# Optimization experiments

Hardware: AMD Instinct MI355X
Metric: run time of the kernel (lower is better)

Reference implementation:

```python
import jax, jax.numpy as jnp
import numpy as np

B, T, D, H = 1, 2048, 1024, 16
HD = D // H
STRIDE = T // 256  # hierarchical global stride (T > 512 branch)


def _mha(q_in, k_in, v_in, Wqkv, bqkv, Wo, bo, nh):
    """torch nn.MultiheadAttention (batch_first, eval/no-dropout), returns (out, head-avg attn)."""
    b, tq, d = q_in.shape
    hd = d // nh
    Wq, Wk, Wv = jnp.split(Wqkv, 3, axis=0)
    bq, bk, bv = jnp.split(bqkv, 3)
    def heads(x, W, bb):
        return (x @ W.T + bb).reshape(b, x.shape[1], nh, hd).transpose(0, 2, 1, 3)
    q = heads(q_in, Wq, bq)
    k = heads(k_in, Wk, bk)
    v = heads(v_in, Wv, bv)
    scores = jnp.einsum('bhtd,bhsd->bhts', q, k) / np.float32(np.sqrt(hd))
    attn = jax.nn.softmax(scores, axis=-1)
    out = jnp.einsum('bhts,bhsd->bhtd', attn, v).transpose(0, 2, 1, 3).reshape(b, tq, d)
    return out @ Wo.T + bo, attn.mean(axis=1)


def _interp_linear(x, size):
    """F.interpolate(mode='linear', align_corners=False) along axis 1. x: [B, Ts, C]."""
    ts = x.shape[1]
    src = (jnp.arange(size, dtype=x.dtype) + 0.5) * (ts / size) - 0.5
    src = jnp.clip(src, 0.0, ts - 1)
    i0 = jnp.floor(src).astype(jnp.int32)
    i1 = jnp.minimum(i0 + 1, ts - 1)
    w = (src - i0.astype(x.dtype))[None, :, None]
    return x[:, i0, :] * (1.0 - w) + x[:, i1, :] * w


def setup_inputs() -> dict:
    rng = jax.random.key(0)
    ks = iter(jax.random.split(rng, 32))
    s = 0.02
    n = lambda shape: jax.random.normal(next(ks), shape, dtype=jnp.float32) * s
    return {
        'query': jax.random.normal(next(ks), (B, T, D), jnp.float32),
        'key': jax.random.normal(next(ks), (B, T, D), jnp.float32),
        'value': jax.random.normal(next(ks), (B, T, D), jnp.float32),
        'strategy_probs': jax.nn.softmax(jax.random.normal(next(ks), (B, 4), jnp.float32), -1),
        'Wqkv_lin': n((3 * D, D)), 'b_lin': jnp.zeros((3 * D,), jnp.float32),
        'Wo_lin': n((D, D)), 'bo_lin': jnp.zeros((D,), jnp.float32),
        'sparsity_pattern': jax.random.normal(next(ks), (H, 1, 1), jnp.float32),
        'Wqkv_loc': n((3 * D, D)), 'b_loc': jnp.zeros((3 * D,), jnp.float32),
        'Wo_loc': n((D, D)), 'bo_loc': jnp.zeros((D,), jnp.float32),
        'Wqkv_glb': n((3 * D, D)), 'b_glb': jnp.zeros((3 * D,), jnp.float32),
        'Wo_glb': n((D, D)), 'bo_glb': jnp.zeros((D,), jnp.float32),
        'Wf': n((D, 2 * D)), 'bf': jnp.zeros((D,), jnp.float32),
        'R_quant': jax.random.normal(next(ks), (H, HD, HD), jnp.float32),
        'ent_gate': jax.random.normal(next(ks), (H, 2, 2), jnp.float32),
    }


def reference(query, key, value, strategy_probs, Wqkv_lin, b_lin, Wo_lin, bo_lin,
              sparsity_pattern, Wqkv_loc, b_loc, Wo_loc, bo_loc,
              Wqkv_glb, b_glb, Wo_glb, bo_glb, Wf, bf, R_quant, ent_gate):
    b, t, d = query.shape
    hd = d // H
    scale = np.float32(np.sqrt(hd))
    # --- 1) "linear" branch: standard MHA ---
    linear_out, linear_w = _mha(query, key, value, Wqkv_lin, b_lin, Wo_lin, bo_lin, H)
    # --- 2) sparse branch (per-head learned on/off mask on raw scores) ---
    qh = query.reshape(b, t, H, hd).transpose(0, 2, 1, 3)
    kh = key.reshape(b, t, H, hd).transpose(0, 2, 1, 3)
    vh = value.reshape(b, t, H, hd).transpose(0, 2, 1, 3)
    scores = jnp.einsum('bhtd,bhsd->bhts', qh, kh) / scale
    mask = (jax.nn.sigmoid(sparsity_pattern) > 0.5).astype(scores.dtype)  # [H,1,1]
    sp_attn = jax.nn.softmax(scores * mask[None], axis=-1)
    sparse_out = jnp.einsum('bhts,bhsd->bhtd', sp_attn, vh).transpose(0, 2, 1, 3).reshape(b, t, d)
    sparse_w = sp_attn.mean(axis=1)
    # --- 3) hierarchical branch (T > 512 path: strided global + linear interp) ---
    local_out, _ = _mha(query, key, value, Wqkv_loc, b_loc, Wo_loc, bo_loc, H // 2)
    gq, gk, gv = query[:, ::STRIDE], key[:, ::STRIDE], value[:, ::STRIDE]
    g_small, _ = _mha(gq, gk, gv, Wqkv_glb, b_glb, Wo_glb, bo_glb, H // 2)
    global_out = _interp_linear(g_small, t)
    hier_out = jnp.concatenate([local_out, global_out], axis=-1) @ Wf.T + bf
    # --- 4) quantum branch (per-head rotation + scalar gate on scores) ---
    q_rot = jnp.einsum('bhtd,hde->bhte', qh, R_quant)
    k_rot = jnp.einsum('bhtd,hde->bhte', kh, R_quant)
    gate = jax.nn.sigmoid(ent_gate[:, 0, 0])[None, :, None, None]  # [1,H,1,1]
    q_attn = jax.nn.softmax((jnp.einsum('bhtd,bhsd->bhts', q_rot, k_rot) / scale) * gate, axis=-1)
    quantum_out = jnp.einsum('bhts,bhsd->bhtd', q_attn, vh).transpose(0, 2, 1, 3).reshape(b, t, d)
    quantum_w = q_attn.mean(axis=1)
    # --- blend via strategy probabilities ---
    sp = strategy_probs[:, :, None]  # [B,4,1]
    all_out = jnp.stack([linear_out, sparse_out, hier_out, quantum_out], axis=1)  # [B,4,T,D]
    weighted = (all_out * sp[..., None]).sum(axis=1)  # [B,T,D]
    wstack = jnp.stack([linear_w, sparse_w, quantum_w], axis=1)  # [B,3,T,T]
    wsel = sp[:, jnp.array([0, 1, 3])][..., None, None]  # [B,3,1,1,1] (faithful to source; requires B==1)
    combined = (wstack * wsel).sum(axis=1)
    return weighted, combined
```

## Files before the change

### kernel.cpp

```cpp
#include <hip/hip_runtime.h>
#include <math.h>

#define D_MODEL 1024

typedef __attribute__((ext_vector_type(8))) short bf16x8;
typedef __attribute__((ext_vector_type(4))) float f32x4;
typedef __attribute__((ext_vector_type(8))) unsigned short u16x8;

__device__ __forceinline__ unsigned short bfr(float f) {
    unsigned u = __float_as_uint(f);
    u += 0x7fffu + ((u >> 16) & 1u);
    return (unsigned short)(u >> 16);
}
__device__ __forceinline__ float bff(unsigned short s) {
    return __uint_as_float(((unsigned)s) << 16);
}
__device__ __forceinline__ void split2(float x, unsigned short &h, unsigned short &l) {
    h = bfr(x);
    l = bfr(x - bff(h));
}
__device__ __forceinline__ unsigned cvtpk(float a, float b) {
    unsigned r;
    asm("v_cvt_pk_bf16_f32 %0, %1, %2" : "=v"(r) : "v"(a), "v"(b));
    return r;
}
__device__ __forceinline__ f32x4 mfma3(bf16x8 ah, bf16x8 al, bf16x8 bh, bf16x8 bl, f32x4 c) {
    c = __builtin_amdgcn_mfma_f32_16x16x32_bf16(ah, bh, c, 0, 0, 0);
    c = __builtin_amdgcn_mfma_f32_16x16x32_bf16(ah, bl, c, 0, 0, 0);
    c = __builtin_amdgcn_mfma_f32_16x16x32_bf16(al, bh, c, 0, 0, 0);
    return c;
}

__global__ __launch_bounds__(256) void split_rm(
    const float* __restrict__ in, unsigned short* __restrict__ hi,
    unsigned short* __restrict__ lo, int n4)
{
    int idx = blockIdx.x * 256 + threadIdx.x;
    if (idx >= n4) return;
    float4 v = ((const float4*)in)[idx];
    ushort4 hs, ls;
    split2(v.x, hs.x, ls.x); split2(v.y, hs.y, ls.y);
    split2(v.z, hs.z, ls.z); split2(v.w, hs.w, ls.w);
    ((ushort4*)hi)[idx] = hs;
    ((ushort4*)lo)[idx] = ls;
}

__global__ __launch_bounds__(256) void split_tr(
    const float* __restrict__ in, unsigned short* __restrict__ hi,
    unsigned short* __restrict__ lo, int T)
{
    __shared__ float xs[64][65];
    const int t0 = blockIdx.x * 64, d0 = blockIdx.y * 64;
    for (int idx = threadIdx.x; idx < 64 * 16; idx += 256) {
        int r = idx >> 4, c4 = (idx & 15) * 4;
        float4 v = *(const float4*)&in[(size_t)(t0 + r) * D_MODEL + d0 + c4];
        xs[r][c4] = v.x; xs[r][c4 + 1] = v.y; xs[r][c4 + 2] = v.z; xs[r][c4 + 3] = v.w;
    }
    __syncthreads();
    for (int idx = threadIdx.x; idx < 64 * 8; idx += 256) {
        int dd = idx >> 3, t8 = (idx & 7) * 8;
        u16x8 hs, ls;
#pragma unroll
        for (int j = 0; j < 8; ++j) {
            unsigned short hh, ll;
            split2(xs[t8 + j][dd], hh, ll);
            hs[j] = hh; ls[j] = ll;
        }
        *(u16x8*)&hi[(size_t)(d0 + dd) * T + t0 + t8] = hs;
        *(u16x8*)&lo[(size_t)(d0 + dd) * T + t0 + t8] = ls;
    }
}

__global__ __launch_bounds__(256) void gemm_mfma(
    const float* __restrict__ X0, const float* __restrict__ X1,
    const float* __restrict__ X2, int xrstride,
    const float* __restrict__ W, size_t wz, int wrstride,
    const float* __restrict__ bias, int bz,
    float* __restrict__ C, size_t cz, int M, int N, int K,
    const float* __restrict__ sptr, int sidx, int accum)
{
    const int z = blockIdx.z;
    const float* X = (z == 0) ? X0 : (z == 1 ? X1 : X2);
    W += (size_t)z * wz;
    if (bias) bias += z * bz;
    C += (size_t)z * cz;

    __shared__ unsigned short Xh[64][40], Xl[64][40];
    __shared__ unsigned short Wh[64][40], Wl[64][40];
    const int tid = threadIdx.x;
    const int m0 = blockIdx.x * 64, n0 = blockIdx.y * 64;
    const int lane = tid & 63, wave = tid >> 6;
    const int c = lane & 15, quad = lane >> 4;
    const int mbase = wave * 16;

    f32x4 acc[4];
#pragma unroll
    for (int nt = 0; nt < 4; ++nt) acc[nt] = (f32x4){0.f, 0.f, 0.f, 0.f};

    float4 xr[2], wr[2];
    const int r_ = tid >> 3, d4_ = (tid & 7) * 4;
    const int r2_ = (tid + 256) >> 3, d42_ = ((tid + 256) & 7) * 4;
    auto ldXW = [&](int k0) {
        xr[0] = *(const float4*)&X[(size_t)(m0 + r_) * xrstride + k0 + d4_];
        xr[1] = *(const float4*)&X[(size_t)(m0 + r2_) * xrstride + k0 + d42_];
        wr[0] = *(const float4*)&W[(size_t)(n0 + r_) * wrstride + k0 + d4_];
        wr[1] = *(const float4*)&W[(size_t)(n0 + r2_) * wrstride + k0 + d42_];
    };
    ldXW(0);

    for (int k0 = 0; k0 < K; k0 += 32) {
        __syncthreads();
        {
            ushort4 hs, ls;
            split2(xr[0].x, hs.x, ls.x); split2(xr[0].y, hs.y, ls.y);
            split2(xr[0].z, hs.z, ls.z); split2(xr[0].w, hs.w, ls.w);
            *(ushort4*)&Xh[r_][d4_] = hs; *(ushort4*)&Xl[r_][d4_] = ls;
            split2(xr[1].x, hs.x, ls.x); split2(xr[1].y, hs.y, ls.y);
            split2(xr[1].z, hs.z, ls.z); split2(xr[1].w, hs.w, ls.w);
            *(ushort4*)&Xh[r2_][d42_] = hs; *(ushort4*)&Xl[r2_][d42_] = ls;
            split2(wr[0].x, hs.x, ls.x); split2(wr[0].y, hs.y, ls.y);
            split2(wr[0].z, hs.z, ls.z); split2(wr[0].w, hs.w, ls.w);
            *(ushort4*)&Wh[r_][d4_] = hs; *(ushort4*)&Wl[r_][d4_] = ls;
            split2(wr[1].x, hs.x, ls.x); split2(wr[1].y, hs.y, ls.y);
            split2(wr[1].z, hs.z, ls.z); split2(wr[1].w, hs.w, ls.w);
            *(ushort4*)&Wh[r2_][d42_] = hs; *(ushort4*)&Wl[r2_][d42_] = ls;
        }
        __syncthreads();
        if (k0 + 32 < K) ldXW(k0 + 32);
        bf16x8 ah = *(const bf16x8*)&Xh[mbase + c][quad * 8];
        bf16x8 al = *(const bf16x8*)&Xl[mbase + c][quad * 8];
#pragma unroll
        for (int nt = 0; nt < 4; ++nt) {
            bf16x8 bh = *(const bf16x8*)&Wh[nt * 16 + c][quad * 8];
            bf16x8 bl = *(const bf16x8*)&Wl[nt * 16 + c][quad * 8];
            acc[nt] = mfma3(ah, al, bh, bl, acc[nt]);
        }
    }
    const float s = (sptr != nullptr) ? sptr[sidx] : 1.0f;
#pragma unroll
    for (int nt = 0; nt < 4; ++nt) {
#pragma unroll
        for (int reg = 0; reg < 4; ++reg) {
            int row = m0 + mbase + quad * 4 + reg;
            int col = n0 + nt * 16 + c;
            float v = acc[nt][reg] + (bias ? bias[col] : 0.0f);
            v *= s;
            size_t gi = (size_t)row * N + col;
            if (accum) v += C[gi];
            C[gi] = v;
        }
    }
}

template <int HD>
__global__ __launch_bounds__(256) void flash_mfma(
    const float* __restrict__ Q,
    const unsigned short* __restrict__ Khi, const unsigned short* __restrict__ Klo,
    const unsigned short* __restrict__ Vthi, const unsigned short* __restrict__ Vtlo,
    const float* __restrict__ aparam, int amode,
    float* __restrict__ O, float* __restrict__ O2,
    const float* __restrict__ strat, int o_sidx, int accum,
    float* __restrict__ mout, float* __restrict__ lout,
    int Tq, int Tk, float inv_scale)
{
    constexpr int ROWS = 64;
    constexpr int STILE = (HD == 64) ? 64 : 32;
    constexpr int MT   = STILE / 16;
    constexpr int KS   = HD / 32;
    constexpr int NT_O = HD / 16;
    constexpr int KS_PV = STILE / 32;
    constexpr bool SWZ = (HD == 64);
    constexpr int KPITCH = SWZ ? HD : HD + 8;
    constexpr int VPITCH = SWZ ? STILE : STILE + 8;
    constexpr int KIT = STILE * HD / 8 / 256;
    constexpr int VIT = STILE * HD / 8 / 256;

    __shared__ __align__(16) unsigned short Kh[STILE * KPITCH], Kl[STILE * KPITCH];
    __shared__ __align__(16) unsigned short Vh[HD * VPITCH],  Vl[HD * VPITCH];
    __shared__ __align__(16) unsigned short Ph[ROWS * VPITCH], Pl[ROWS * VPITCH];

    auto KIX = [](int r, int cc) {
        return SWZ ? r * HD + ((cc & 7) | ((((cc >> 3) ^ r) & 7) << 3))
                   : r * KPITCH + cc;
    };
    auto VIX = [](int d, int s) {
        return SWZ ? d * STILE + ((s & 7) | ((((s >> 3) ^ d) & 7) << 3))
                   : d * VPITCH + s;
    };
    auto PIX = [](int r, int cc) {
        return SWZ ? r * STILE + ((cc & 7) | ((((cc >> 3) ^ r) & 7) << 3))
                   : r * VPITCH + cc;
    };

    const int tid = threadIdx.x;
    const int h = blockIdx.y;
    const int r0 = blockIdx.x * ROWS;
    const int lane = tid & 63, wave = tid >> 6;
    const int c = lane & 15, quad = lane >> 4;
    const int mbase = wave * 16;
    const int ZS = gridDim.z;
    const int tkloc = Tk / ZS;
    const int kv0 = blockIdx.z * tkloc;

    float gate = 1.0f;
    if (amode == 1) gate = (aparam[h] > 0.0f) ? 1.0f : 0.0f;
    if (amode == 2) gate = 1.0f / (1.0f + __expf(-aparam[h * 4]));
    const float ascale = gate * inv_scale;
    const bool masked = (amode == 1) && (gate == 0.0f);

    bf16x8 qah[KS], qal[KS];
    if (!masked) {
        const float* qrow = &Q[(size_t)(r0 + mbase + c) * D_MODEL + h * HD];
#pragma unroll
        for (int ks = 0; ks < KS; ++ks) {
            float4 a  = *(const float4*)(qrow + ks * 32 + quad * 8);
            float4 b2 = *(const float4*)(qrow + ks * 32 + quad * 8 + 4);
            unsigned short hh, ll;
            split2(a.x, hh, ll);  qah[ks][0] = (short)hh; qal[ks][0] = (short)ll;
            split2(a.y, hh, ll);  qah[ks][1] = (short)hh; qal[ks][1] = (short)ll;
            split2(a.z, hh, ll);  qah[ks][2] = (short)hh; qal[ks][2] = (short)ll;
            split2(a.w, hh, ll);  qah[ks][3] = (short)hh; qal[ks][3] = (short)ll;
            split2(b2.x, hh, ll); qah[ks][4] = (short)hh; qal[ks][4] = (short)ll;
            split2(b2.y, hh, ll); qah[ks][5] = (short)hh; qal[ks][5] = (short)ll;
            split2(b2.z, hh, ll); qah[ks][6] = (short)hh; qal[ks][6] = (short)ll;
            split2(b2.w, hh, ll); qah[ks][7] = (short)hh; qal[ks][7] = (short)ll;
        }
    }

    float mreg = -1e30f, lacc = 0.0f;
    f32x4 oacc[NT_O];
#pragma unroll
    for (int nt = 0; nt < NT_O; ++nt) oacc[nt] = (f32x4){0.f, 0.f, 0.f, 0.f};

    bf16x8 pone, pzero;
#pragma unroll
    for (int j = 0; j < 8; ++j) { pone[j] = (short)0x3F80; pzero[j] = 0; }

    u16x8 krh[KIT], krl[KIT], vrh[VIT], vrl[VIT];

    auto load_regs = [&](int s0) {
        if (!masked) {
#pragma unroll
            for (int it = 0; it < KIT; ++it) {
                int idx = tid + it * 256;
                int r = idx / (HD / 8), c8 = (idx % (HD / 8)) * 8;
                size_t go = (size_t)(s0 + r) * D_MODEL + h * HD + c8;
                krh[it] = *(const u16x8*)&Khi[go];
                krl[it] = *(const u16x8*)&Klo[go];
            }
        }
#pragma unroll
        for (int it = 0; it < VIT; ++it) {
            int idx = tid + it * 256;
            int d = idx % HD, s8 = (idx / HD) * 8;
            size_t go = (size_t)(h * HD + d) * Tk + s0 + s8;
            vrh[it] = *(const u16x8*)&Vthi[go];
            vrl[it] = *(const u16x8*)&Vtlo[go];
        }
    };
    auto write_bufs = [&]() {
        if (!masked) {
#pragma unroll
            for (int it = 0; it < KIT; ++it) {
                int idx = tid + it * 256;
                int r = idx / (HD / 8), c8 = (idx % (HD / 8)) * 8;
                *(u16x8*)&Kh[KIX(r, c8)] = krh[it];
                *(u16x8*)&Kl[KIX(r, c8)] = krl[it];
            }
        }
#pragma unroll
        for (int it = 0; it < VIT; ++it) {
            int idx = tid + it * 256;
            int d = idx % HD, s8 = (idx / HD) * 8;
            *(u16x8*)&Vh[VIX(d, s8)] = vrh[it];
            *(u16x8*)&Vl[VIX(d, s8)] = vrl[it];
        }
    };

    auto compute_tile = [&]() {
        if (!masked) {
            f32x4 sf[MT];
#pragma unroll
            for (int mt = 0; mt < MT; ++mt) {
                f32x4 s = (f32x4){0.f, 0.f, 0.f, 0.f};
#pragma unroll
                for (int ks = 0; ks < KS; ++ks) {
                    bf16x8 kh = *(const bf16x8*)&Kh[KIX(mt * 16 + c, ks * 32 + quad * 8)];
                    bf16x8 kl = *(const bf16x8*)&Kl[KIX(mt * 16 + c, ks * 32 + quad * 8)];
                    s = mfma3(kh, kl, qah[ks], qal[ks], s);
                }
                sf[mt] = s * ascale;
            }
            float tm = sf[0][0];
#pragma unroll
            for (int mt = 0; mt < MT; ++mt)
#pragma unroll
                for (int reg = 0; reg < 4; ++reg) tm = fmaxf(tm, sf[mt][reg]);
            if (__any(tm > mreg + 8.0f)) {
                tm = fmaxf(tm, __shfl_xor(tm, 16));
                tm = fmaxf(tm, __shfl_xor(tm, 32));
                float nm = fmaxf(mreg, tm);
                float al = __expf(mreg - nm);
                mreg = nm;
                lacc *= al;
                float ar[4];
#pragma unroll
                for (int reg = 0; reg < 4; ++reg)
                    ar[reg] = __shfl(al, (lane & 48) | (quad * 4 + reg));
#pragma unroll
                for (int nt = 0; nt < NT_O; ++nt)
#pragma unroll
                    for (int reg = 0; reg < 4; ++reg) oacc[nt][reg] *= ar[reg];
            }
#pragma unroll
            for (int mt = 0; mt < MT; ++mt) {
                float p0 = __expf(sf[mt][0] - mreg);
                float p1 = __expf(sf[mt][1] - mreg);
                float p2 = __expf(sf[mt][2] - mreg);
                float p3 = __expf(sf[mt][3] - mreg);
                lacc += (p0 + p1) + (p2 + p3);
                unsigned h01 = cvtpk(p0, p1), h23 = cvtpk(p2, p3);
                float b0 = __uint_as_float(h01 << 16);
                float b1 = __uint_as_float(h01 & 0xffff0000u);
                float b2 = __uint_as_float(h23 << 16);
                float b3 = __uint_as_float(h23 & 0xffff0000u);
                unsigned l01 = cvtpk(p0 - b0, p1 - b1);
                unsigned l23 = cvtpk(p2 - b2, p3 - b3);
                uint2 hw; hw.x = h01; hw.y = h23;
                uint2 lw; lw.x = l01; lw.y = l23;
                *(uint2*)&Ph[PIX(mbase + c, mt * 16 + quad * 4)] = hw;
                *(uint2*)&Pl[PIX(mbase + c, mt * 16 + quad * 4)] = lw;
            }
        }
        bf16x8 pah[KS_PV], pal[KS_PV];
#pragma unroll
        for (int ks = 0; ks < KS_PV; ++ks) {
            if (masked) { pah[ks] = pone; pal[ks] = pzero; }
            else {
                pah[ks] = *(const bf16x8*)&Ph[PIX(mbase + c, ks * 32 + quad * 8)];
                pal[ks] = *(const bf16x8*)&Pl[PIX(mbase + c, ks * 32 + quad * 8)];
            }
        }
#pragma unroll
        for (int nt = 0; nt < NT_O; ++nt) {
            f32x4 o = oacc[nt];
#pragma unroll
            for (int ks = 0; ks < KS_PV; ++ks) {
                bf16x8 bh = *(const bf16x8*)&Vh[VIX(nt * 16 + c, ks * 32 + quad * 8)];
                bf16x8 bl = *(const bf16x8*)&Vl[VIX(nt * 16 + c, ks * 32 + quad * 8)];
                o = mfma3(pah[ks], pal[ks], bh, bl, o);
            }
            oacc[nt] = o;
        }
    };

    const int NTL = tkloc / STILE;
    load_regs(kv0);
    for (int t = 0; t < NTL; ++t) {
        __syncthreads();
        write_bufs();
        __syncthreads();
        if (t + 1 < NTL) load_regs(kv0 + (t + 1) * STILE);
        compute_tile();
    }

    lacc += __shfl_xor(lacc, 16);
    lacc += __shfl_xor(lacc, 32);

    if (ZS == 1) {
        const float osc = (o_sidx >= 0) ? strat[o_sidx] : 1.0f;
        if (quad == 0) {
            int row = r0 + mbase + c;
            mout[h * Tq + row] = masked ? 0.0f : mreg;
            lout[h * Tq + row] = masked ? (float)Tk : lacc;
        }
        float sc[4];
#pragma unroll
        for (int reg = 0; reg < 4; ++reg) {
            float lf = masked ? (float)Tk
                              : __shfl(lacc, (lane & 48) | (quad * 4 + reg));
            sc[reg] = osc / lf;
        }
#pragma unroll
        for (int reg = 0; reg < 4; ++reg) {
            int row = r0 + mbase + quad * 4 + reg;
#pragma unroll
            for (int nt = 0; nt < NT_O; ++nt) {
                size_t gi = (size_t)row * D_MODEL + h * HD + nt * 16 + c;
                float v = sc[reg] * oacc[nt][reg];
                if (accum) v += O[gi];
                O[gi] = v;
            }
        }
    } else {
        float* Op = (blockIdx.z == 0) ? O : O2;
        if (quad == 0) {
            int row = r0 + mbase + c;
            mout[(blockIdx.z * gridDim.y + h) * Tq + row] = masked ? 0.0f : mreg;
            lout[(blockIdx.z * gridDim.y + h) * Tq + row] = masked ? (float)tkloc : lacc;
        }
#pragma unroll
        for (int reg = 0; reg < 4; ++reg) {
            int row = r0 + mbase + quad * 4 + reg;
#pragma unroll
            for (int nt = 0; nt < NT_O; ++nt)
                Op[(size_t)row * D_MODEL + h * HD + nt * 16 + c] = oacc[nt][reg];
        }
    }
}

__global__ __launch_bounds__(256) void combineK(
    const float* __restrict__ O0, const float* __restrict__ O1,
    const float* __restrict__ mp, const float* __restrict__ lp,
    float* __restrict__ O, float* __restrict__ mf, float* __restrict__ lf,
    const float* __restrict__ strat, int o_sidx, int accum, int Tq,
    int hdshift, int NH)
{
    const int row = blockIdx.x;
    const int c4 = threadIdx.x * 4;
    const int h = c4 >> hdshift;
    const float m0 = mp[h * Tq + row], m1 = mp[(NH + h) * Tq + row];
    const float l0 = lp[h * Tq + row], l1 = lp[(NH + h) * Tq + row];
    const float m = fmaxf(m0, m1);
    const float w0 = __expf(m0 - m), w1 = __expf(m1 - m);
    const float lsum = l0 * w0 + l1 * w1;
    if (mf && (c4 & ((1 << hdshift) - 1)) == 0) {
        mf[h * Tq + row] = m;
        lf[h * Tq + row] = lsum;
    }
    const float osc = (o_sidx >= 0) ? strat[o_sidx] : 1.0f;
    const float sc = osc / lsum;
    float4 a = *(const float4*)&O0[(size_t)row * D_MODEL + c4];
    float4 b = *(const float4*)&O1[(size_t)row * D_MODEL + c4];
    size_t gi = (size_t)row * D_MODEL + c4;
    float4 r;
    r.x = sc * (a.x * w0 + b.x * w1);
    r.y = sc * (a.y * w0 + b.y * w1);
    r.z = sc * (a.z * w0 + b.z * w1);
    r.w = sc * (a.w * w0 + b.w * w1);
    if (accum) {
        float4 o = *(const float4*)&O[gi];
        r.x += o.x; r.y += o.y; r.z += o.z; r.w += o.w;
    }
    *(float4*)&O[gi] = r;
}

__global__ __launch_bounds__(256) void comb_mfma(
    const unsigned short* __restrict__ Qhi, const unsigned short* __restrict__ Qlo,
    const unsigned short* __restrict__ Khi, const unsigned short* __restrict__ Klo,
    const float* __restrict__ mrow, const float* __restrict__ lrow,
    const float* __restrict__ aparam, int amode,
    const float* __restrict__ strat,
    float* __restrict__ comb, int Tq, int Tk, int nh, float inv_scale)
{
    __shared__ __align__(16) unsigned short Kh[128][72], Kl[128][72];
    __shared__ float msh[16 * 64], lsh[16 * 64];
    const int tid = threadIdx.x;
    const int r0 = blockIdx.x * 64, c0 = blockIdx.y * 128;
    const int lane = tid & 63, wave = tid >> 6;
    const int c = lane & 15, quad = lane >> 4;
    const int mbase = wave * 16;

    for (int idx = tid; idx < nh * 64; idx += 256) {
        int hh = idx >> 6, rr = idx & 63;
        msh[idx] = mrow[hh * Tq + r0 + rr];
        lsh[idx] = 1.0f / lrow[hh * Tq + r0 + rr];
    }

    f32x4 acc[8];
#pragma unroll
    for (int nt = 0; nt < 8; ++nt) acc[nt] = (f32x4){0.f, 0.f, 0.f, 0.f};

    int hlist[16]; float glist[16]; int nact = 0; float unif = 0.0f;
    for (int h = 0; h < nh; ++h) {
        float gate = 1.0f;
        if (amode == 1) gate = (aparam[h] > 0.0f) ? 1.0f : 0.0f;
        if (amode == 2) gate = 1.0f / (1.0f + __expf(-aparam[h * 4]));
        if (amode == 1 && gate == 0.0f) { unif += 1.0f; continue; }
        hlist[nact] = h; glist[nact] = gate * inv_scale; ++nact;
    }

    u16x8 krh[4], krl[4];
    auto loadK = [&](int h) {
#pragma unroll
        for (int it = 0; it < 4; ++it) {
            int idx = tid + it * 256;
            int r = idx >> 3, c8 = (idx & 7) * 8;
            size_t go = (size_t)(c0 + r) * D_MODEL + h * 64 + c8;
            krh[it] = *(const u16x8*)&Khi[go];
            krl[it] = *(const u16x8*)&Klo[go];
        }
    };
    if (nact > 0) loadK(hlist[0]);

    for (int i = 0; i < nact; ++i) {
        const int h = hlist[i];
        const float ascale = glist[i];
        __syncthreads();
#pragma unroll
        for (int it = 0; it < 4; ++it) {
            int idx = tid + it * 256;
            int r = idx >> 3, c8 = (idx & 7) * 8;
            *(u16x8*)&Kh[r][c8] = krh[it];
            *(u16x8*)&Kl[r][c8] = krl[it];
        }
        __syncthreads();
        if (i + 1 < nact) loadK(hlist[i + 1]);

        bf16x8 qah[2], qal[2];
        const unsigned short* qh = &Qhi[(size_t)(r0 + mbase + c) * D_MODEL + h * 64];
        const unsigned short* ql = &Qlo[(size_t)(r0 + mbase + c) * D_MODEL + h * 64];
#pragma unroll
        for (int ks = 0; ks < 2; ++ks) {
            qah[ks] = *(const bf16x8*)(qh + ks * 32 + quad * 8);
            qal[ks] = *(const bf16x8*)(ql + ks * 32 + quad * 8);
        }

        float mr[4], li[4];
#pragma unroll
        for (int reg = 0; reg < 4; ++reg) {
            mr[reg] = msh[h * 64 + mbase + quad * 4 + reg];
            li[reg] = lsh[h * 64 + mbase + quad * 4 + reg];
        }
#pragma unroll
        for (int nt = 0; nt < 8; ++nt) {
            f32x4 s = (f32x4){0.f, 0.f, 0.f, 0.f};
#pragma unroll
            for (int ks = 0; ks < 2; ++ks) {
                bf16x8 bh = *(const bf16x8*)&Kh[nt * 16 + c][ks * 32 + quad * 8];
                bf16x8 bl = *(const bf16x8*)&Kl[nt * 16 + c][ks * 32 + quad * 8];
                s = mfma3(qah[ks], qal[ks], bh, bl, s);
            }
#pragma unroll
            for (int reg = 0; reg < 4; ++reg)
                acc[nt][reg] += __expf(s[reg] * ascale - mr[reg]) * li[reg];
        }
    }
    const float csc = (strat[0] + strat[1] + strat[3]) / (float)nh;
    const float uadd = unif / (float)Tk;
#pragma unroll
    for (int nt = 0; nt < 8; ++nt) {
#pragma unroll
        for (int reg = 0; reg < 4; ++reg) {
            int row = r0 + mbase + quad * 4 + reg;
            comb[(size_t)row * Tk + c0 + nt * 16 + c] = csc * (acc[nt][reg] + uadd);
        }
    }
}

__global__ __launch_bounds__(256) void rotate_heads(
    const float* __restrict__ X0, const float* __restrict__ X1,
    const float* __restrict__ R,
    float* __restrict__ Y0, float* __restrict__ Y1)
{
    const float* X = blockIdx.z ? X1 : X0;
    float* Y = blockIdx.z ? Y1 : Y0;
    __shared__ float Rt[64][68];
    __shared__ float xs[64][68];
    const int tid = threadIdx.x;
    const int h = blockIdx.y;
    const int t0 = blockIdx.x * 64;
    for (int idx = tid; idx < 4096; idx += 256) {
        int d = idx >> 6, e = idx & 63;
        Rt[e][d] = R[h * 4096 + idx];
        xs[d][e] = X[(size_t)(t0 + d) * D_MODEL + h * 64 + e];
    }
    __syncthreads();
    const int ty = tid >> 4, tx = tid & 15;
    float acc[4][4] = {};
#pragma unroll 4
    for (int d0 = 0; d0 < 64; d0 += 4) {
        float4 rv[4];
#pragma unroll
        for (int j = 0; j < 4; ++j) rv[j] = *(const float4*)&Rt[tx * 4 + j][d0];
#pragma unroll
        for (int i = 0; i < 4; ++i) {
            float4 a = *(const float4*)&xs[ty * 4 + i][d0];
#pragma unroll
            for (int j = 0; j < 4; ++j)
                acc[i][j] += a.x * rv[j].x + a.y * rv[j].y + a.z * rv[j].z + a.w * rv[j].w;
        }
    }
#pragma unroll
    for (int i = 0; i < 4; ++i)
#pragma unroll
        for (int j = 0; j < 4; ++j)
            Y[(size_t)(t0 + ty * 4 + i) * D_MODEL + h * 64 + tx * 4 + j] = acc[i][j];
}

__global__ __launch_bounds__(256) void interp_lin(
    const float* __restrict__ G, float* __restrict__ out)
{
    const int t = blockIdx.x;
    float src = (t + 0.5f) * 0.125f - 0.5f;
    src = fminf(fmaxf(src, 0.0f), 255.0f);
    float fl = floorf(src);
    int i0 = (int)fl;
    int i1 = min(i0 + 1, 255);
    float w = src - fl;
    const float4* g0 = (const float4*)(G + (size_t)i0 * D_MODEL);
    const float4* g1 = (const float4*)(G + (size_t)i1 * D_MODEL);
    float4* o = (float4*)(out + (size_t)t * D_MODEL);
    int c = threadIdx.x;
    float4 a = g0[c], b = g1[c];
    float4 r;
    r.x = a.x * (1.0f - w) + b.x * w;
    r.y = a.y * (1.0f - w) + b.y * w;
    r.z = a.z * (1.0f - w) + b.z * w;
    r.w = a.w * (1.0f - w) + b.w * w;
    o[c] = r;
}

extern "C" void kernel_launch(void* const* d_in, const int* in_sizes, int n_in,
                              void* d_out, int out_size, void* d_ws, size_t ws_size,
                              hipStream_t stream)
{
    (void)in_sizes; (void)n_in; (void)ws_size; (void)out_size;
    const float* query    = (const float*)d_in[0];
    const float* key      = (const float*)d_in[1];
    const float* value    = (const float*)d_in[2];
    const float* strat    = (const float*)d_in[3];
    const float* Wqkv_lin = (const float*)d_in[4];
    const float* b_lin    = (const float*)d_in[5];
    const float* Wo_lin   = (const float*)d_in[6];
    const float* bo_lin   = (const float*)d_in[7];
    const float* spars    = (const float*)d_in[8];
    const float* Wqkv_loc = (const float*)d_in[9];
    const float* b_loc    = (const float*)d_in[10];
    const float* Wo_loc   = (const float*)d_in[11];
    const float* bo_loc   = (const float*)d_in[12];
    const float* Wqkv_glb = (const float*)d_in[13];
    const float* b_glb    = (const float*)d_in[14];
    const float* Wo_glb   = (const float*)d_in[15];
    const float* bo_glb   = (const float*)d_in[16];
    const float* Wf       = (const float*)d_in[17];
    const float* bf       = (const float*)d_in[18];
    const float* Rq       = (const float*)d_in[19];
    const float* ent      = (const float*)d_in[20];

    float* out = (float*)d_out;
    float* weighted = out;
    float* combined = out + (size_t)2048 * 1024;
    const size_t PLANE = (size_t)2048 * 2048;

    float* ws   = (float*)d_ws;
    float* qkv  = ws;
    float* AO   = qkv + 6291456;
    float* LO   = AO + 2097152;
    float* gqkv = LO + 2097152;
    float* gAO  = gqkv + 786432;
    float* gOUT = gAO + 262144;
    float* GI   = gOUT + 262144;
    float* mb   = GI + 2097152;
    float* lb   = mb + 65536;
    float* qrot = qkv;
    float* krot = qkv + 2097152;
    unsigned short* Ksp_h = (unsigned short*)(lb + 65536);
    unsigned short* Ksp_l = Ksp_h + 2097152;
    unsigned short* Vtp_h = Ksp_l + 2097152;
    unsigned short* Vtp_l = Vtp_h + 2097152;
    unsigned short* gKs_h = Vtp_l + 2097152;
    unsigned short* gKs_l = gKs_h + 262144;
    unsigned short* gVt_h = gKs_l + 262144;
    unsigned short* gVt_l = gVt_h + 262144;
    float* mc = (float*)(gVt_l + 262144);
    float* lc = mc + 32768;
    unsigned short* Qsp_h = (unsigned short*)GI;
    unsigned short* Qsp_l = Qsp_h + 2097152;

    const float inv8   = 0.125f;
    const float inv128 = 1.0f / sqrtf(128.0f);

    hipMemsetAsync(weighted, 0, (size_t)2097152 * sizeof(float), stream);

    gemm_mfma<<<dim3(32, 16, 3), 256, 0, stream>>>(
        query, key, value, 1024, Wqkv_lin, 1048576, 1024, b_lin, 1024,
        qkv, 2097152, 2048, 1024, 1024, nullptr, 0, 0);
    split_rm<<<dim3(2048), 256, 0, stream>>>(qkv + 2097152, Ksp_h, Ksp_l, 524288);
    split_tr<<<dim3(32, 16), 256, 0, stream>>>(qkv + 4194304, Vtp_h, Vtp_l, 2048);
    flash_mfma<64><<<dim3(32, 16, 2), 256, 0, stream>>>(
        qkv, Ksp_h, Ksp_l, Vtp_h, Vtp_l, nullptr, 0,
        AO, GI, strat, -1, 0, mb, lb, 2048, 2048, inv8);
    combineK<<<dim3(2048), 256, 0, stream>>>(
        AO, GI, mb, lb, AO, mc, lc, strat, -1, 0, 2048, 6, 16);
    split_rm<<<dim3(2048), 256, 0, stream>>>(qkv, Qsp_h, Qsp_l, 524288);
    comb_mfma<<<dim3(32, 16), 256, 0, stream>>>(
        Qsp_h, Qsp_l, Ksp_h, Ksp_l, mc, lc, nullptr, 0, strat,
        combined + 0 * PLANE, 2048, 2048, 16, inv8);
    gemm_mfma<<<dim3(32, 16, 1), 256, 0, stream>>>(
        AO, AO, AO, 1024, Wo_lin, 0, 1024, bo_lin, 0,
        weighted, 0, 2048, 1024, 1024, strat, 0, 1);

    split_rm<<<dim3(2048), 256, 0, stream>>>(key, Ksp_h, Ksp_l, 524288);
    split_tr<<<dim3(32, 16), 256, 0, stream>>>(value, Vtp_h, Vtp_l, 2048);
    flash_mfma<64><<<dim3(32, 16, 2), 256, 0, stream>>>(
        query, Ksp_h, Ksp_l, Vtp_h, Vtp_l, spars, 1,
        AO, GI, strat, 1, 1, mb, lb, 2048, 2048, inv8);
    combineK<<<dim3(2048), 256, 0, stream>>>(
        AO, GI, mb, lb, weighted, mc, lc, strat, 1, 1, 2048, 6, 16);
    split_rm<<<dim3(2048), 256, 0, stream>>>(query, Qsp_h, Qsp_l, 524288);
    comb_mfma<<<dim3(32, 16), 256, 0, stream>>>(
        Qsp_h, Qsp_l, Ksp_h, Ksp_l, mc, lc, spars, 1, strat,
        combined + 1 * PLANE, 2048, 2048, 16, inv8);

    rotate_heads<<<dim3(32, 16, 2), 256, 0, stream>>>(query, key, Rq, qrot, krot);
    split_rm<<<dim3(2048), 256, 0, stream>>>(krot, Ksp_h, Ksp_l, 524288);
    flash_mfma<64><<<dim3(32, 16, 2), 256, 0, stream>>>(
        qrot, Ksp_h, Ksp_l, Vtp_h, Vtp_l, ent, 2,
        AO, GI, strat, 3, 1, mb, lb, 2048, 2048, inv8);
    combineK<<<dim3(2048), 256, 0, stream>>>(
        AO, GI, mb, lb, weighted, mc, lc, strat, 3, 1, 2048, 6, 16);
    split_rm<<<dim3(2048), 256, 0, stream>>>(qrot, Qsp_h, Qsp_l, 524288);
    comb_mfma<<<dim3(32, 16), 256, 0, stream>>>(
        Qsp_h, Qsp_l, Ksp_h, Ksp_l, mc, lc, ent, 2, strat,
        combined + 2 * PLANE, 2048, 2048, 16, inv8);

    gemm_mfma<<<dim3(32, 16, 3), 256, 0, stream>>>(
        query, key, value, 1024, Wqkv_loc, 1048576, 1024, b_loc, 1024,
        qkv, 2097152, 2048, 1024, 1024, nullptr, 0, 0);
    split_rm<<<dim3(2048), 256, 0, stream>>>(qkv + 2097152, Ksp_h, Ksp_l, 524288);
    split_tr<<<dim3(32, 16), 256, 0, stream>>>(qkv + 4194304, Vtp_h, Vtp_l, 2048);
    flash_mfma<128><<<dim3(32, 8, 2), 256, 0, stream>>>(
        qkv, Ksp_h, Ksp_l, Vtp_h, Vtp_l, nullptr, 0,
        AO, GI, strat, -1, 0, mb, lb, 2048, 2048, inv128);
    combineK<<<dim3(2048), 256, 0, stream>>>(
        AO, GI, mb, lb, AO, nullptr, nullptr, strat, -1, 0, 2048, 7, 8);
    gemm_mfma<<<dim3(32, 16, 1), 256, 0, stream>>>(
        AO, AO, AO, 1024, Wo_loc, 0, 1024, bo_loc, 0,
        LO, 0, 2048, 1024, 1024, nullptr, 0, 0);

    gemm_mfma<<<dim3(4, 16, 3), 256, 0, stream>>>(
        query, key, value, 8192, Wqkv_glb, 1048576, 1024, b_glb, 1024,
        gqkv, 262144, 256, 1024, 1024, nullptr, 0, 0);
    split_rm<<<dim3(256), 256, 0, stream>>>(gqkv + 262144, gKs_h, gKs_l, 65536);
    split_tr<<<dim3(4, 16), 256, 0, stream>>>(gqkv + 524288, gVt_h, gVt_l, 256);
    flash_mfma<128><<<dim3(4, 8, 1), 256, 0, stream>>>(
        gqkv, gKs_h, gKs_l, gVt_h, gVt_l, nullptr, 0,
        gAO, nullptr, strat, -1, 0, mb, lb, 256, 256, inv128);
    gemm_mfma<<<dim3(4, 16, 1), 256, 0, stream>>>(
        gAO, gAO, gAO, 1024, Wo_glb, 0, 1024, bo_glb, 0,
        gOUT, 0, 256, 1024, 1024, nullptr, 0, 0);
    interp_lin<<<dim3(2048), 256, 0, stream>>>(gOUT, GI);

    gemm_mfma<<<dim3(32, 16, 1), 256, 0, stream>>>(
        LO, LO, LO, 1024, Wf, 0, 2048, bf, 0,
        weighted, 0, 2048, 1024, 1024, strat, 2, 1);
    gemm_mfma<<<dim3(32, 16, 1), 256, 0, stream>>>(
        GI, GI, GI, 1024, Wf + 1024, 0, 2048, nullptr, 0,
        weighted, 0, 2048, 1024, 1024, strat, 2, 1);
}
```

Before: 1.078 ms.

## Pre-split GEMM operands into bf16 hi/lo once and reuse across branches

The GEMM kernel now loads pre-split bf16 hi/lo operands instead of fp32 data that it had to split into hi/lo inside every tile iteration. Query, key and value are split once and the results are shared by the three QKV projections, and also stand in for the separate key/query splits in the sparse branch. Weights and activations are split by extra split_rm launches before each GEMM. This removes redundant per-tile conversion work but adds several kernel launches and extra global traffic to write and read the split buffers.

New measurement: 1.035 ms. 1.04x faster.

```diff
diff --git a/kernel.cpp b/kernel.cpp
--- a/kernel.cpp
+++ b/kernel.cpp
@@ -71,22 +71,26 @@
     }
 }
 
-__global__ __launch_bounds__(256) void gemm_mfma(
-    const float* __restrict__ X0, const float* __restrict__ X1,
-    const float* __restrict__ X2, int xrstride,
-    const float* __restrict__ W, size_t wz, int wrstride,
+__global__ __launch_bounds__(256) void gemm_bf(
+    const unsigned short* __restrict__ Xh0, const unsigned short* __restrict__ Xl0,
+    const unsigned short* __restrict__ Xh1, const unsigned short* __restrict__ Xl1,
+    const unsigned short* __restrict__ Xh2, const unsigned short* __restrict__ Xl2,
+    int xrstride,
+    const unsigned short* __restrict__ Whi, const unsigned short* __restrict__ Wlo,
+    size_t wz, int wrstride,
     const float* __restrict__ bias, int bz,
     float* __restrict__ C, size_t cz, int M, int N, int K,
     const float* __restrict__ sptr, int sidx, int accum)
 {
     const int z = blockIdx.z;
-    const float* X = (z == 0) ? X0 : (z == 1 ? X1 : X2);
-    W += (size_t)z * wz;
+    const unsigned short* Xh_g = (z == 0) ? Xh0 : (z == 1 ? Xh1 : Xh2);
+    const unsigned short* Xl_g = (z == 0) ? Xl0 : (z == 1 ? Xl1 : Xl2);
+    Whi += (size_t)z * wz; Wlo += (size_t)z * wz;
     if (bias) bias += z * bz;
     C += (size_t)z * cz;
 
-    __shared__ unsigned short Xh[64][40], Xl[64][40];
-    __shared__ unsigned short Wh[64][40], Wl[64][40];
+    __shared__ __align__(16) unsigned short Xh[64][40], Xl[64][40];
+    __shared__ __align__(16) unsigned short Wh[64][40], Wl[64][40];
     const int tid = threadIdx.x;
     const int m0 = blockIdx.x * 64, n0 = blockIdx.y * 64;
     const int lane = tid & 63, wave = tid >> 6;
@@ -97,36 +101,26 @@
 #pragma unroll
     for (int nt = 0; nt < 4; ++nt) acc[nt] = (f32x4){0.f, 0.f, 0.f, 0.f};
 
-    float4 xr[2], wr[2];
-    const int r_ = tid >> 3, d4_ = (tid & 7) * 4;
-    const int r2_ = (tid + 256) >> 3, d42_ = ((tid + 256) & 7) * 4;
-    auto ldXW = [&](int k0) {
-        xr[0] = *(const float4*)&X[(size_t)(m0 + r_) * xrstride + k0 + d4_];
-        xr[1] = *(const float4*)&X[(size_t)(m0 + r2_) * xrstride + k0 + d42_];
-        wr[0] = *(const float4*)&W[(size_t)(n0 + r_) * wrstride + k0 + d4_];
-        wr[1] = *(const float4*)&W[(size_t)(n0 + r2_) * wrstride + k0 + d42_];
+    const int r_ = tid >> 2, c8_ = (tid & 3) * 8;
+    u16x8 xh, xl, wh, wl;
+    auto ld = [&](int k0) {
+        size_t xo = (size_t)(m0 + r_) * xrstride + k0 + c8_;
+        xh = *(const u16x8*)&Xh_g[xo];
+        xl = *(const u16x8*)&Xl_g[xo];
+        size_t wo = (size_t)(n0 + r_) * wrstride + k0 + c8_;
+        wh = *(const u16x8*)&Whi[wo];
+        wl = *(const u16x8*)&Wlo[wo];
     };
-    ldXW(0);
+    ld(0);
 
     for (int k0 = 0; k0 < K; k0 += 32) {
         __syncthreads();
-        {
-            ushort4 hs, ls;
-            split2(xr[0].x, hs.x, ls.x); split2(xr[0].y, hs.y, ls.y);
-            split2(xr[0].z, hs.z, ls.z); split2(xr[0].w, hs.w, ls.w);
-            *(ushort4*)&Xh[r_][d4_] = hs; *(ushort4*)&Xl[r_][d4_] = ls;
-            split2(xr[1].x, hs.x, ls.x); split2(xr[1].y, hs.y, ls.y);
-            split2(xr[1].z, hs.z, ls.z); split2(xr[1].w, hs.w, ls.w);
-            *(ushort4*)&Xh[r2_][d42_] = hs; *(ushort4*)&Xl[r2_][d42_] = ls;
-            split2(wr[0].x, hs.x, ls.x); split2(wr[0].y, hs.y, ls.y);
-            split2(wr[0].z, hs.z, ls.z); split2(wr[0].w, hs.w, ls.w);
-            *(ushort4*)&Wh[r_][d4_] = hs; *(ushort4*)&Wl[r_][d4_] = ls;
-            split2(wr[1].x, hs.x, ls.x); split2(wr[1].y, hs.y, ls.y);
-            split2(wr[1].z, hs.z, ls.z); split2(wr[1].w, hs.w, ls.w);
-            *(ushort4*)&Wh[r2_][d42_] = hs; *(ushort4*)&Wl[r2_][d42_] = ls;
-        }
+        *(u16x8*)&Xh[r_][c8_] = xh;
+        *(u16x8*)&Xl[r_][c8_] = xl;
+        *(u16x8*)&Wh[r_][c8_] = wh;
+        *(u16x8*)&Wl[r_][c8_] = wl;
         __syncthreads();
-        if (k0 + 32 < K) ldXW(k0 + 32);
+        if (k0 + 32 < K) ld(k0 + 32);
         bf16x8 ah = *(const bf16x8*)&Xh[mbase + c][quad * 8];
         bf16x8 al = *(const bf16x8*)&Xl[mbase + c][quad * 8];
 #pragma unroll
@@ -665,6 +659,16 @@
     unsigned short* gVt_l = gVt_h + 262144;
     float* mc = (float*)(gVt_l + 262144);
     float* lc = mc + 32768;
+    unsigned short* Iq_h = (unsigned short*)(lc + 32768);
+    unsigned short* Iq_l = Iq_h + 2097152;
+    unsigned short* Ik_h = Iq_l + 2097152;
+    unsigned short* Ik_l = Ik_h + 2097152;
+    unsigned short* Iv_h = Ik_l + 2097152;
+    unsigned short* Iv_l = Iv_h + 2097152;
+    unsigned short* Wsp_h = Iv_l + 2097152;
+    unsigned short* Wsp_l = Wsp_h + 3145728;
+    unsigned short* Asp_h = (unsigned short*)qkv;
+    unsigned short* Asp_l = Asp_h + 2097152;
     unsigned short* Qsp_h = (unsigned short*)GI;
     unsigned short* Qsp_l = Qsp_h + 2097152;
 
@@ -673,8 +677,14 @@
 
     hipMemsetAsync(weighted, 0, (size_t)2097152 * sizeof(float), stream);
 
-    gemm_mfma<<<dim3(32, 16, 3), 256, 0, stream>>>(
-        query, key, value, 1024, Wqkv_lin, 1048576, 1024, b_lin, 1024,
+    split_rm<<<dim3(2048), 256, 0, stream>>>(query, Iq_h, Iq_l, 524288);
+    split_rm<<<dim3(2048), 256, 0, stream>>>(key,   Ik_h, Ik_l, 524288);
+    split_rm<<<dim3(2048), 256, 0, stream>>>(value, Iv_h, Iv_l, 524288);
+
+    split_rm<<<dim3(3072), 256, 0, stream>>>(Wqkv_lin, Wsp_h, Wsp_l, 786432);
+    gemm_bf<<<dim3(32, 16, 3), 256, 0, stream>>>(
+        Iq_h, Iq_l, Ik_h, Ik_l, Iv_h, Iv_l, 1024,
+        Wsp_h, Wsp_l, 1048576, 1024, b_lin, 1024,
         qkv, 2097152, 2048, 1024, 1024, nullptr, 0, 0);
     split_rm<<<dim3(2048), 256, 0, stream>>>(qkv + 2097152, Ksp_h, Ksp_l, 524288);
     split_tr<<<dim3(32, 16), 256, 0, stream>>>(qkv + 4194304, Vtp_h, Vtp_l, 2048);
@@ -687,20 +697,21 @@
     comb_mfma<<<dim3(32, 16), 256, 0, stream>>>(
         Qsp_h, Qsp_l, Ksp_h, Ksp_l, mc, lc, nullptr, 0, strat,
         combined + 0 * PLANE, 2048, 2048, 16, inv8);
-    gemm_mfma<<<dim3(32, 16, 1), 256, 0, stream>>>(
-        AO, AO, AO, 1024, Wo_lin, 0, 1024, bo_lin, 0,
+    split_rm<<<dim3(2048), 256, 0, stream>>>(AO, Asp_h, Asp_l, 524288);
+    split_rm<<<dim3(1024), 256, 0, stream>>>(Wo_lin, Wsp_h, Wsp_l, 262144);
+    gemm_bf<<<dim3(32, 16, 1), 256, 0, stream>>>(
+        Asp_h, Asp_l, Asp_h, Asp_l, Asp_h, Asp_l, 1024,
+        Wsp_h, Wsp_l, 0, 1024, bo_lin, 0,
         weighted, 0, 2048, 1024, 1024, strat, 0, 1);
 
-    split_rm<<<dim3(2048), 256, 0, stream>>>(key, Ksp_h, Ksp_l, 524288);
     split_tr<<<dim3(32, 16), 256, 0, stream>>>(value, Vtp_h, Vtp_l, 2048);
     flash_mfma<64><<<dim3(32, 16, 2), 256, 0, stream>>>(
-        query, Ksp_h, Ksp_l, Vtp_h, Vtp_l, spars, 1,
+        query, Ik_h, Ik_l, Vtp_h, Vtp_l, spars, 1,
         AO, GI, strat, 1, 1, mb, lb, 2048, 2048, inv8);
     combineK<<<dim3(2048), 256, 0, stream>>>(
         AO, GI, mb, lb, weighted, mc, lc, strat, 1, 1, 2048, 6, 16);
-    split_rm<<<dim3(2048), 256, 0, stream>>>(query, Qsp_h, Qsp_l, 524288);
     comb_mfma<<<dim3(32, 16), 256, 0, stream>>>(
-        Qsp_h, Qsp_l, Ksp_h, Ksp_l, mc, lc, spars, 1, strat,
+        Iq_h, Iq_l, Ik_h, Ik_l, mc, lc, spars, 1, strat,
         combined + 1 * PLANE, 2048, 2048, 16, inv8);
 
     rotate_heads<<<dim3(32, 16, 2), 256, 0, stream>>>(query, key, Rq, qrot, krot);
@@ -715,8 +726,10 @@
         Qsp_h, Qsp_l, Ksp_h, Ksp_l, mc, lc, ent, 2, strat,
         combined + 2 * PLANE, 2048, 2048, 16, inv8);
 
-    gemm_mfma<<<dim3(32, 16, 3), 256, 0, stream>>>(
-        query, key, value, 1024, Wqkv_loc, 1048576, 1024, b_loc, 1024,
+    split_rm<<<dim3(3072), 256, 0, stream>>>(Wqkv_loc, Wsp_h, Wsp_l, 786432);
+    gemm_bf<<<dim3(32, 16, 3), 256, 0, stream>>>(
+        Iq_h, Iq_l, Ik_h, Ik_l, Iv_h, Iv_l, 1024,
+        Wsp_h, Wsp_l, 1048576, 1024, b_loc, 1024,
         qkv, 2097152, 2048, 1024, 1024, nullptr, 0, 0);
     split_rm<<<dim3(2048), 256, 0, stream>>>(qkv + 2097152, Ksp_h, Ksp_l, 524288);
     split_tr<<<dim3(32, 16), 256, 0, stream>>>(qkv + 4194304, Vtp_h, Vtp_l, 2048);
@@ -725,27 +738,40 @@
         AO, GI, strat, -1, 0, mb, lb, 2048, 2048, inv128);
     combineK<<<dim3(2048), 256, 0, stream>>>(
         AO, GI, mb, lb, AO, nullptr, nullptr, strat, -1, 0, 2048, 7, 8);
-    gemm_mfma<<<dim3(32, 16, 1), 256, 0, stream>>>(
-        AO, AO, AO, 1024, Wo_loc, 0, 1024, bo_loc, 0,
+    split_rm<<<dim3(2048), 256, 0, stream>>>(AO, Asp_h, Asp_l, 524288);
+    split_rm<<<dim3(1024), 256, 0, stream>>>(Wo_loc, Wsp_h, Wsp_l, 262144);
+    gemm_bf<<<dim3(32, 16, 1), 256, 0, stream>>>(
+        Asp_h, Asp_l, Asp_h, Asp_l, Asp_h, Asp_l, 1024,
+        Wsp_h, Wsp_l, 0, 1024, bo_loc, 0,
         LO, 0, 2048, 1024, 1024, nullptr, 0, 0);
 
-    gemm_mfma<<<dim3(4, 16, 3), 256, 0, stream>>>(
-        query, key, value, 8192, Wqkv_glb, 1048576, 1024, b_glb, 1024,
+    split_rm<<<dim3(3072), 256, 0, stream>>>(Wqkv_glb, Wsp_h, Wsp_l, 786432);
+    gemm_bf<<<dim3(4, 16, 3), 256, 0, stream>>>(
+        Iq_h, Iq_l, Ik_h, Ik_l, Iv_h, Iv_l, 8192,
+        Wsp_h, Wsp_l, 1048576, 1024, b_glb, 1024,
         gqkv, 262144, 256, 1024, 1024, nullptr, 0, 0);
     split_rm<<<dim3(256), 256, 0, stream>>>(gqkv + 262144, gKs_h, gKs_l, 65536);
     split_tr<<<dim3(4, 16), 256, 0, stream>>>(gqkv + 524288, gVt_h, gVt_l, 256);
     flash_mfma<128><<<dim3(4, 8, 1), 256, 0, stream>>>(
         gqkv, gKs_h, gKs_l, gVt_h, gVt_l, nullptr, 0,
         gAO, nullptr, strat, -1, 0, mb, lb, 256, 256, inv128);
-    gemm_mfma<<<dim3(4, 16, 1), 256, 0, stream>>>(
-        gAO, gAO, gAO, 1024, Wo_glb, 0, 1024, bo_glb, 0,
+    split_rm<<<dim3(256), 256, 0, stream>>>(gAO, Asp_h, Asp_l, 65536);
+    split_rm<<<dim3(1024), 256, 0, stream>>>(Wo_glb, Wsp_h, Wsp_l, 262144);
+    gemm_bf<<<dim3(4, 16, 1), 256, 0, stream>>>(
+        Asp_h, Asp_l, Asp_h, Asp_l, Asp_h, Asp_l, 1024,
+        Wsp_h, Wsp_l, 0, 1024, bo_glb, 0,
         gOUT, 0, 256, 1024, 1024, nullptr, 0, 0);
     interp_lin<<<dim3(2048), 256, 0, stream>>>(gOUT, GI);
 
-    gemm_mfma<<<dim3(32, 16, 1), 256, 0, stream>>>(
-        LO, LO, LO, 1024, Wf, 0, 2048, bf, 0,
+    split_rm<<<dim3(2048), 256, 0, stream>>>(Wf, Wsp_h, Wsp_l, 524288);
+    split_rm<<<dim3(2048), 256, 0, stream>>>(LO, Asp_h, Asp_l, 524288);
+    gemm_bf<<<dim3(32, 16, 1), 256, 0, stream>>>(
+        Asp_h, Asp_l, Asp_h, Asp_l, Asp_h, Asp_l, 1024,
+        Wsp_h, Wsp_l, 0, 2048, bf, 0,
         weighted, 0, 2048, 1024, 1024, strat, 2, 1);
-    gemm_mfma<<<dim3(32, 16, 1), 256, 0, stream>>>(
-        GI, GI, GI, 1024, Wf + 1024, 0, 2048, nullptr, 0,
+    split_rm<<<dim3(2048), 256, 0, stream>>>(GI, Asp_h, Asp_l, 524288);
+    gemm_bf<<<dim3(32, 16, 1), 256, 0, stream>>>(
+        Asp_h, Asp_l, Asp_h, Asp_l, Asp_h, Asp_l, 1024,
+        Wsp_h + 1024, Wsp_l + 1024, 0, 2048, nullptr, 0,
         weighted, 0, 2048, 1024, 1024, strat, 2, 1);
 }
```
